# Optimization experiments

Hardware: AMD Instinct MI355X
Metric: run time of the kernel (lower is better)

The kernel has to match this reference:

```python
import jax, jax.numpy as jnp
import numpy as np

MIN_BIN_WIDTH = 1e-3
MIN_BIN_HEIGHT = 1e-3
MIN_DERIVATIVE = 1e-3
TAIL_BOUND = 1.0
N_POS = 2097152
N_CHANNELS = 8
N_BINS = 128
DEFAULT_INIT = float(np.log(np.exp(1.0 - MIN_DERIVATIVE) - 1.0))


def setup_inputs() -> dict:
    key = jax.random.key(0)
    k1, k2, k3, k4 = jax.random.split(key, 4)
    # positions rescaled to roughly [-1, 1]; include slight tail overshoot
    x = jax.random.uniform(k1, (N_POS, N_CHANNELS), minval=-1.1, maxval=1.1, dtype=jnp.float32)
    uw = DEFAULT_INIT + 0.1 * jax.random.normal(k2, (N_CHANNELS, N_BINS), dtype=jnp.float32)
    uh = DEFAULT_INIT + 0.1 * jax.random.normal(k3, (N_CHANNELS, N_BINS), dtype=jnp.float32)
    ud = DEFAULT_INIT + 0.1 * jax.random.normal(k4, (N_CHANNELS, N_BINS - 1), dtype=jnp.float32)
    return {"x": x, "unnormalized_widths": uw, "unnormalized_heights": uh,
            "unnormalized_derivatives": ud}


def _bin_edges(unnormalized, min_size, left, right):
    # softmax-normalized sizes with a minimum bin size, cumsum -> knot locations
    n_bins = unnormalized.shape[-1]
    sizes = jax.nn.softmax(unnormalized, axis=-1)
    sizes = min_size + (1.0 - min_size * n_bins) * sizes
    cum = jnp.cumsum(sizes, axis=-1)
    cum = jnp.pad(cum, ((0, 0), (1, 0)))
    cum = (right - left) * cum + left
    cum = cum.at[..., 0].set(left).at[..., -1].set(right)
    sizes = cum[..., 1:] - cum[..., :-1]
    return sizes, cum


def _log_prob(x, uw, uh, ud):
    left, right = -TAIL_BOUND, TAIL_BOUND
    bottom, top = -TAIL_BOUND, TAIL_BOUND
    C = uw.shape[0]

    widths, cumwidths = _bin_edges(uw * 10.0, MIN_BIN_WIDTH, left, right)      # (C,B),(C,B+1)
    heights, cumheights = _bin_edges(uh * 10.0, MIN_BIN_HEIGHT, bottom, top)   # (C,B),(C,B+1)
    ud_pad = jnp.pad(ud, ((0, 0), (1, 1)), constant_values=DEFAULT_INIT)       # linear tails
    derivatives = MIN_DERIVATIVE + jax.nn.softplus(ud_pad)                      # (C,B+1)
    delta = heights / widths                                                    # (C,B)

    inside = (x >= left) & (x <= right)
    xc = jnp.clip(x, bottom, top)  # inverse pass searches over cumheights

    edges = cumheights.at[:, -1].add(1e-6)
    # per-channel bin search, memory-light searchsorted
    idx = jax.vmap(lambda e, v: jnp.searchsorted(e, v, side='right'),
                   in_axes=(0, 1), out_axes=1)(edges, xc) - 1                   # (N,C)
    idx = jnp.clip(idx, 0, widths.shape[-1] - 1)

    ch = jnp.arange(C)[None, :]
    icw = cumwidths[ch, idx]
    ibw = widths[ch, idx]
    ich = cumheights[ch, idx]
    ih = heights[ch, idx]
    idl = delta[ch, idx]
    d0 = derivatives[ch, idx]
    d1 = derivatives[ch, idx + 1]

    # quadratic inverse solve (Durkan et al. rational-quadratic spline)
    dy = xc - ich
    t = d0 + d1 - 2.0 * idl
    a = dy * t + ih * (idl - d0)
    b = ih * d0 - dy * t
    c = -idl * dy
    disc = jnp.maximum(b * b - 4.0 * a * c, 0.0)
    root = (2.0 * c) / (-b - jnp.sqrt(disc))
    theta_1m = root * (1.0 - root)
    denom = idl + t * theta_1m
    der_num = (idl ** 2) * (d1 * root ** 2 + 2.0 * idl * theta_1m + d0 * (1.0 - root) ** 2)
    logabsdet = jnp.log(der_num) - 2.0 * jnp.log(denom)
    logdet = jnp.where(inside, -logabsdet, 0.0)  # identity tails -> logdet 0
    return np.log(0.5).astype(np.float32) + logdet


def reference(x, unnormalized_widths, unnormalized_heights, unnormalized_derivatives):
    return _log_prob(x, unnormalized_widths, unnormalized_heights, unnormalized_derivatives)
```

## Files before the change

kernel.cpp:

```cpp
#include <hip/hip_runtime.h>
#include <math.h>


#define NB 128
#define NCH 8
#define NSLOT 1024
#define PACK_B 4128
#define HINT_B 16416
#define TAB_FLOATS 6152

typedef float v2f __attribute__((ext_vector_type(2)));

static __device__ inline unsigned short f2h(float v) {
    union { _Float16 h; unsigned short u; } c;
    c.h = (_Float16)v;
    return c.u;
}
static __device__ inline float h16lo(unsigned u) {
    union { unsigned short s; _Float16 h; } c; c.s = (unsigned short)(u & 0xffffu);
    return (float)c.h;
}
static __device__ inline float h16hi(unsigned u) {
    union { unsigned short s; _Float16 h; } c; c.s = (unsigned short)(u >> 16);
    return (float)c.h;
}

__global__ __launch_bounds__(128) void spline_precompute(
    const float* __restrict__ uw, const float* __restrict__ uh,
    const float* __restrict__ ud, float* __restrict__ ws)
{
    const int c = blockIdx.x;
    const int i = threadIdx.x;
    __shared__ float red[128];
    __shared__ float scan[128];
    __shared__ float cum[129];
    __shared__ float wdt[128];
    __shared__ float sdv[129];
    const float DEFAULT_INIT = logf(expf(1.0f - 1e-3f) - 1.0f);

    float v = uw[c * NB + i] * 10.0f;
    red[i] = v; __syncthreads();
    #pragma unroll
    for (int s = 64; s >= 1; s >>= 1) { if (i < s) red[i] = fmaxf(red[i], red[i + s]); __syncthreads(); }
    float ex = expf(v - red[0]);
    __syncthreads();
    red[i] = ex; __syncthreads();
    #pragma unroll
    for (int s = 64; s >= 1; s >>= 1) { if (i < s) red[i] += red[i + s]; __syncthreads(); }
    float sz = 1e-3f + (1.0f - 1e-3f * NB) * (ex / red[0]);
    __syncthreads();
    scan[i] = sz;
    for (int off = 1; off < NB; off <<= 1) {
        __syncthreads();
        float t = (i >= off) ? scan[i - off] : 0.0f;
        __syncthreads();
        scan[i] += t;
    }
    __syncthreads();
    if (i == 0) cum[0] = -1.0f;
    cum[i + 1] = (i == NB - 1) ? 1.0f : fmaf(2.0f, scan[i], -1.0f);
    __syncthreads();
    wdt[i] = cum[i + 1] - cum[i];
    __syncthreads();

    v = uh[c * NB + i] * 10.0f;
    red[i] = v; __syncthreads();
    #pragma unroll
    for (int s = 64; s >= 1; s >>= 1) { if (i < s) red[i] = fmaxf(red[i], red[i + s]); __syncthreads(); }
    ex = expf(v - red[0]);
    __syncthreads();
    red[i] = ex; __syncthreads();
    #pragma unroll
    for (int s = 64; s >= 1; s >>= 1) { if (i < s) red[i] += red[i + s]; __syncthreads(); }
    sz = 1e-3f + (1.0f - 1e-3f * NB) * (ex / red[0]);
    __syncthreads();
    scan[i] = sz;
    for (int off = 1; off < NB; off <<= 1) {
        __syncthreads();
        float t = (i >= off) ? scan[i - off] : 0.0f;
        __syncthreads();
        scan[i] += t;
    }
    __syncthreads();
    if (i == 0) cum[0] = -1.0f;
    cum[i + 1] = (i == NB - 1) ? 1.0f : fmaf(2.0f, scan[i], -1.0f);

    float u0 = (i == 0) ? DEFAULT_INIT : ud[c * (NB - 1) + i - 1];
    sdv[i] = 1e-3f + log1pf(expf(u0));
    if (i == NB - 1) sdv[NB] = 1e-3f + log1pf(expf(DEFAULT_INIT));
    __syncthreads();

    float hh  = cum[i + 1] - cum[i];
    float idl = hh / wdt[i];
    float d0v = sdv[i], d1v = sdv[i + 1];
    float Tv  = d0v + d1v - 2.0f * idl;

    ws[c * 129 + i] = cum[i];
    if (i == NB - 1) ws[c * 129 + NB] = 1.0f + 1e-6f;

    unsigned* g_pk = reinterpret_cast<unsigned*>(reinterpret_cast<char*>(ws) + PACK_B);
    const int pw = (c * NB + i) * 3;
    g_pk[pw]     = __float_as_uint(hh);
    g_pk[pw + 1] = (unsigned)f2h(idl) | ((unsigned)f2h(d0v) << 16);
    g_pk[pw + 2] = (unsigned)f2h(Tv);

    unsigned char* g_hint = reinterpret_cast<unsigned char*>(ws) + HINT_B;
    for (int s = i; s < NSLOT; s += NB) {
        float left = (float)s * (2.0f / NSLOT) - 1.0f;
        int k = 0;
        #pragma unroll
        for (int st = 64; st >= 1; st >>= 1) {
            int t = k + st;
            if (cum[t] <= left) k = t;
        }
        g_hint[c * NSLOT + s] = (unsigned char)k;
    }
}

__global__ __launch_bounds__(256, 6) void spline_main(
    const float4* __restrict__ x4, float4* __restrict__ out4,
    const float* __restrict__ ws, int npair)
{
    __shared__ __align__(16) float tab[TAB_FLOATS];
    {
        float4* dst = reinterpret_cast<float4*>(tab);
        const float4* src = reinterpret_cast<const float4*>(ws);
        for (int t = threadIdx.x; t < TAB_FLOATS / 4; t += 256) dst[t] = src[t];
    }
    __syncthreads();
    const float* eg = tab;
    const unsigned* pku = reinterpret_cast<const unsigned*>(
        reinterpret_cast<const char*>(tab) + PACK_B);
    const unsigned char* hint = reinterpret_cast<const unsigned char*>(tab) + HINT_B;

    const float LOG_HALF = -0.6931471805599453f;
    const float LN2 = 0.6931471805599453f;
    const int tid = blockIdx.x * 256 + threadIdx.x;
    const int stride = gridDim.x * 256;

    float4 pfa, pfb;
    if (tid < npair) { pfa = x4[2 * tid]; pfb = x4[2 * tid + 1]; }

    for (int i = tid; i < npair; i += stride) {
        float4 xa = pfa, xb = pfb;
        int inx = i + stride;
        inx = (inx < npair) ? inx : i;
        pfa = x4[2 * inx];
        pfb = x4[2 * inx + 1];

        float xs[8] = {xa.x, xa.y, xa.z, xa.w, xb.x, xb.y, xb.z, xb.w};

        float xq[8];
        int kk[8];
        #pragma unroll
        for (int j = 0; j < 8; ++j) {
            float xc = __builtin_amdgcn_fmed3f(xs[j], -1.0f, 1.0f);
            xq[j] = xc;
            int s = (int)fmaf(xc, (float)(NSLOT / 2), (float)(NSLOT / 2));
            s = (s > NSLOT - 1) ? NSLOT - 1 : s;
            kk[j] = hint[j * NSLOT + s];
        }

        float e0[8], e1[8];
        #pragma unroll
        for (int j = 0; j < 8; ++j) {
            const float* ej = eg + j * 129 + kk[j];
            e0[j] = ej[0];
            e1[j] = ej[1];
        }

        unsigned pw0[8], pw1[8], pw2[8];
        float dyv[8], lm[8];
        #pragma unroll
        for (int j = 0; j < 8; ++j) {
            bool adv = (e1[j] <= xq[j]);
            int k2 = kk[j] + (adv ? 1 : 0);
            float elo = adv ? e1[j] : e0[j];
            dyv[j] = xq[j] - elo;
            lm[j] = (xs[j] == xq[j]) ? LN2 : 0.0f;
            const unsigned* p = pku + (j * NB + k2) * 3;
            pw0[j] = p[0];
            pw1[j] = p[1];
            pw2[j] = p[2];
        }

        float rs[8];
        #pragma unroll
        for (int jj = 0; jj < 4; ++jj) {
            v2f h  = {__uint_as_float(pw0[jj]), __uint_as_float(pw0[jj + 4])};
            v2f dl = {h16lo(pw1[jj]), h16lo(pw1[jj + 4])};
            v2f d0 = {h16hi(pw1[jj]), h16hi(pw1[jj + 4])};
            v2f T  = {h16lo(pw2[jj]), h16lo(pw2[jj + 4])};
            v2f dy = {dyv[jj], dyv[jj + 4]};
            const v2f four = {4.0f, 4.0f};
            const v2f zz = {0.0f, 0.0f};

            v2f dyt  = dy * T;
            v2f sdd  = dl - d0;
            v2f a    = __builtin_elementwise_fma(h, sdd, dyt);
            v2f b    = __builtin_elementwise_fma(h, d0, -dyt);
            v2f cp   = dl * dy;
            v2f ac   = a * cp;
            v2f disc = __builtin_elementwise_max(
                           __builtin_elementwise_fma(four, ac, b * b), zz);
            v2f sq   = {__builtin_amdgcn_sqrtf(disc.x),
                        __builtin_amdgcn_sqrtf(disc.y)};
            v2f t2   = b + sq;
            v2f uu   = cp + cp;
            v2f t2s  = t2 * t2;
            v2f tu   = T * uu;
            v2f tmu  = t2 - uu;
            v2f denb = __builtin_elementwise_fma(tu, tmu, dl * t2s);
            v2f numf = h * denb;
            v2f den  = (dl * sq) * t2s;

            float la = __log2f(numf.x) - __log2f(den.x);
            float lb = __log2f(numf.y) - __log2f(den.y);
            rs[jj]     = fmaf(lm[jj],     la, LOG_HALF);
            rs[jj + 4] = fmaf(lm[jj + 4], lb, LOG_HALF);
        }

        out4[2 * i]     = make_float4(rs[0], rs[1], rs[2], rs[3]);
        out4[2 * i + 1] = make_float4(rs[4], rs[5], rs[6], rs[7]);
    }
}

extern "C" void kernel_launch(void* const* d_in, const int* in_sizes, int n_in,
                              void* d_out, int out_size, void* d_ws, size_t ws_size,
                              hipStream_t stream) {
    const float* x  = (const float*)d_in[0];
    const float* uw = (const float*)d_in[1];
    const float* uh = (const float*)d_in[2];
    const float* ud = (const float*)d_in[3];
    float* ws = (float*)d_ws;

    spline_precompute<<<NCH, NB, 0, stream>>>(uw, uh, ud, ws);

    const int npair = out_size / 8;
    spline_main<<<2048, 256, 0, stream>>>(
        (const float4*)x, (float4*)d_out, ws, npair);
}
```

Measured before the change: 40.05 us.

## Resolve bin with fine-grained hint split and interleaved per-bin records

```diff
diff --git a/kernel.cpp b/kernel.cpp
--- a/kernel.cpp
+++ b/kernel.cpp
@@ -5,16 +5,15 @@
 #define NB 128
 #define NCH 8
 #define NSLOT 1024
-#define PACK_B 4128
-#define HINT_B 16416
-#define TAB_FLOATS 6152
+#define HINT_B 20640
+#define TAB_FLOATS 9256
 
 typedef float v2f __attribute__((ext_vector_type(2)));
 
-static __device__ inline unsigned short f2h(float v) {
+static __device__ inline unsigned f2h(float v) {
     union { _Float16 h; unsigned short u; } c;
     c.h = (_Float16)v;
-    return c.u;
+    return (unsigned)c.u;
 }
 static __device__ inline float h16lo(unsigned u) {
     union { unsigned short s; _Float16 h; } c; c.s = (unsigned short)(u & 0xffffu);
@@ -95,16 +94,24 @@
     float d0v = sdv[i], d1v = sdv[i + 1];
     float Tv  = d0v + d1v - 2.0f * idl;
 
-    ws[c * 129 + i] = cum[i];
-    if (i == NB - 1) ws[c * 129 + NB] = 1.0f + 1e-6f;
-
-    unsigned* g_pk = reinterpret_cast<unsigned*>(reinterpret_cast<char*>(ws) + PACK_B);
-    const int pw = (c * NB + i) * 3;
-    g_pk[pw]     = __float_as_uint(hh);
-    g_pk[pw + 1] = (unsigned)f2h(idl) | ((unsigned)f2h(d0v) << 16);
-    g_pk[pw + 2] = (unsigned)f2h(Tv);
-
-    unsigned char* g_hint = reinterpret_cast<unsigned char*>(ws) + HINT_B;
+    unsigned* g_rec = reinterpret_cast<unsigned*>(ws);
+    const int rw = (c * 129 + i) * 5;
+    g_rec[rw]     = __float_as_uint(cum[i]);
+    g_rec[rw + 1] = __float_as_uint(hh);
+    g_rec[rw + 2] = f2h(idl) | (f2h(d0v) << 16);
+    g_rec[rw + 3] = f2h(Tv);
+    g_rec[rw + 4] = 0u;
+    if (i == NB - 1) {
+        const int pw = (c * 129 + NB) * 5;
+        g_rec[pw]     = __float_as_uint(1.0f);
+        g_rec[pw + 1] = __float_as_uint(1.0f);
+        g_rec[pw + 2] = f2h(1.0f) | (f2h(1.0f) << 16);
+        g_rec[pw + 3] = 0u;
+        g_rec[pw + 4] = 0u;
+    }
+
+    unsigned short* g_hint = reinterpret_cast<unsigned short*>(
+        reinterpret_cast<char*>(ws) + HINT_B);
     for (int s = i; s < NSLOT; s += NB) {
         float left = (float)s * (2.0f / NSLOT) - 1.0f;
         int k = 0;
@@ -113,11 +120,14 @@
             int t = k + st;
             if (cum[t] <= left) k = t;
         }
-        g_hint[c * NSLOT + s] = (unsigned char)k;
-    }
-}
-
-__global__ __launch_bounds__(256, 6) void spline_main(
+        float X = (cum[k + 1] - left) * 262144.0f;
+        int split = (int)ceilf(X) - 1;
+        split = split < 0 ? 0 : (split > 511 ? 511 : split);
+        g_hint[c * NSLOT + s] = (unsigned short)(k | (split << 7));
+    }
+}
+
+__global__ __launch_bounds__(256, 4) void spline_main(
     const float4* __restrict__ x4, float4* __restrict__ out4,
     const float* __restrict__ ws, int npair)
 {
@@ -128,10 +138,9 @@
         for (int t = threadIdx.x; t < TAB_FLOATS / 4; t += 256) dst[t] = src[t];
     }
     __syncthreads();
-    const float* eg = tab;
-    const unsigned* pku = reinterpret_cast<const unsigned*>(
-        reinterpret_cast<const char*>(tab) + PACK_B);
-    const unsigned char* hint = reinterpret_cast<const unsigned char*>(tab) + HINT_B;
+    const unsigned* rec = reinterpret_cast<const unsigned*>(tab);
+    const unsigned short* hint = reinterpret_cast<const unsigned short*>(
+        reinterpret_cast<const char*>(tab) + HINT_B);
 
     const float LOG_HALF = -0.6931471805599453f;
     const float LN2 = 0.6931471805599453f;
@@ -151,50 +160,46 @@
         float xs[8] = {xa.x, xa.y, xa.z, xa.w, xb.x, xb.y, xb.z, xb.w};
 
         float xq[8];
-        int kk[8];
+        int qv[8];
+        unsigned hv[8];
         #pragma unroll
         for (int j = 0; j < 8; ++j) {
             float xc = __builtin_amdgcn_fmed3f(xs[j], -1.0f, 1.0f);
             xq[j] = xc;
-            int s = (int)fmaf(xc, (float)(NSLOT / 2), (float)(NSLOT / 2));
-            s = (s > NSLOT - 1) ? NSLOT - 1 : s;
-            kk[j] = hint[j * NSLOT + s];
-        }
-
-        float e0[8], e1[8];
+            float g = fmaf(xc, 262144.0f, 262144.0f);
+            int gi = (int)g;
+            gi = gi > 524287 ? 524287 : gi;
+            qv[j] = gi & 511;
+            hv[j] = hint[j * NSLOT + (gi >> 9)];
+        }
+
+        unsigned p0[8], p1[8], p2[8], p3[8];
         #pragma unroll
         for (int j = 0; j < 8; ++j) {
-            const float* ej = eg + j * 129 + kk[j];
-            e0[j] = ej[0];
-            e1[j] = ej[1];
-        }
-
-        unsigned pw0[8], pw1[8], pw2[8];
-        float dyv[8], lm[8];
-        #pragma unroll
-        for (int j = 0; j < 8; ++j) {
-            bool adv = (e1[j] <= xq[j]);
-            int k2 = kk[j] + (adv ? 1 : 0);
-            float elo = adv ? e1[j] : e0[j];
-            dyv[j] = xq[j] - elo;
-            lm[j] = (xs[j] == xq[j]) ? LN2 : 0.0f;
-            const unsigned* p = pku + (j * NB + k2) * 3;
-            pw0[j] = p[0];
-            pw1[j] = p[1];
-            pw2[j] = p[2];
+            int k2 = (int)(hv[j] & 127u) + ((qv[j] > (int)(hv[j] >> 7)) ? 1 : 0);
+            const unsigned* p = rec + (j * 129 + k2) * 5;
+            p0[j] = p[0];
+            p1[j] = p[1];
+            p2[j] = p[2];
+            p3[j] = p[3];
         }
 
         float rs[8];
         #pragma unroll
         for (int jj = 0; jj < 4; ++jj) {
-            v2f h  = {__uint_as_float(pw0[jj]), __uint_as_float(pw0[jj + 4])};
-            v2f dl = {h16lo(pw1[jj]), h16lo(pw1[jj + 4])};
-            v2f d0 = {h16hi(pw1[jj]), h16hi(pw1[jj + 4])};
-            v2f T  = {h16lo(pw2[jj]), h16lo(pw2[jj + 4])};
-            v2f dy = {dyv[jj], dyv[jj + 4]};
+            v2f el = {__uint_as_float(p0[jj]), __uint_as_float(p0[jj + 4])};
+            v2f h  = {__uint_as_float(p1[jj]), __uint_as_float(p1[jj + 4])};
+            v2f dl = {h16lo(p2[jj]), h16lo(p2[jj + 4])};
+            v2f d0 = {h16hi(p2[jj]), h16hi(p2[jj + 4])};
+            v2f T  = {h16lo(p3[jj]), h16lo(p3[jj + 4])};
+            v2f xv = {xq[jj], xq[jj + 4]};
+            v2f xr = {xs[jj], xs[jj + 4]};
             const v2f four = {4.0f, 4.0f};
             const v2f zz = {0.0f, 0.0f};
 
+            v2f dyr  = xv - el;
+            v2f dy   = {__builtin_amdgcn_fmed3f(dyr.x, 0.0f, h.x),
+                        __builtin_amdgcn_fmed3f(dyr.y, 0.0f, h.y)};
             v2f dyt  = dy * T;
             v2f sdd  = dl - d0;
             v2f a    = __builtin_elementwise_fma(h, sdd, dyt);
@@ -216,8 +221,10 @@
 
             float la = __log2f(numf.x) - __log2f(den.x);
             float lb = __log2f(numf.y) - __log2f(den.y);
-            rs[jj]     = fmaf(lm[jj],     la, LOG_HALF);
-            rs[jj + 4] = fmaf(lm[jj + 4], lb, LOG_HALF);
+            float lma = (xr.x == xv.x) ? LN2 : 0.0f;
+            float lmb = (xr.y == xv.y) ? LN2 : 0.0f;
+            rs[jj]     = fmaf(lma, la, LOG_HALF);
+            rs[jj + 4] = fmaf(lmb, lb, LOG_HALF);
         }
 
         out4[2 * i]     = make_float4(rs[0], rs[1], rs[2], rs[3]);
```

Measured after the change: 39.99 us. Within noise of the previous version (-0.1%).
